# Kernel optimization log

Measured on AMD Instinct MI355X. Metric: run time of the kernel, lower is better.

## Reference

```python
import jax, jax.numpy as jnp
import numpy as np

WINDOW = 12  # fixed half-window from the original module


def setup_inputs() -> dict:
    key = jax.random.key(0)
    ks = jax.random.split(key, 8)
    B, S, G, H = 8, 512, 16, 128
    Da, Dm = 8 * H, 2 * H
    att = jax.random.normal(ks[0], (B, S, Da), jnp.float32)
    mod = jax.random.normal(ks[1], (B, S, Dm), jnp.float32)
    W_att = jax.random.normal(ks[2], (3 * Da,), jnp.float32) * 0.02
    b_att = jax.random.normal(ks[3], (1,), jnp.float32) * 0.02
    W_mod = jax.random.normal(ks[4], (3 * Dm,), jnp.float32) * 0.02
    b_mod = jax.random.normal(ks[5], (1,), jnp.float32) * 0.02
    q_enc = jax.random.normal(ks[6], (B, 30, Dm), jnp.float32)
    gap_indices = jax.random.randint(ks[7], (B, G), 0, S)
    mask = jnp.ones((B, S), jnp.int32)
    q_mask = jnp.ones((B, 30), jnp.int32)
    return dict(att=att, mod=mod, W_att=W_att, b_att=b_att, W_mod=W_mod,
                b_mod=b_mod, q_enc=q_enc, gap_indices=gap_indices,
                mask=mask, q_mask=q_mask)


def _pools(x, maskf, wmf):
    # x: [B,S,D]; maskf: [B,S] float; wmf: [B,G-1,S] float window masks
    # gap 0: full-sequence pooling (max is unmasked, avg divides by mask sum -- faithful)
    max0 = jnp.max(x, axis=1)                                   # [B,D]
    avg0 = jnp.sum(x, axis=1) / jnp.sum(maskf, axis=1, keepdims=True)
    p0 = jnp.concatenate([max0, avg0], axis=-1)[:, None, :]      # [B,1,2D]
    # remaining gaps: masked windowed max/avg (masked entries zeroed, as in torch)
    s = jnp.einsum('bgs,bsd->bgd', wmf, x)                       # windowed sums
    cnt = jnp.sum(wmf, axis=2, keepdims=True)                    # [B,G-1,1]
    avg = s / cnt
    mx = jnp.max(x[:, None, :, :] * wmf[:, :, :, None], axis=2)  # [B,G-1,D]
    return jnp.concatenate([p0, jnp.concatenate([mx, avg], axis=-1)], axis=1)


def reference(att, mod, W_att, b_att, W_mod, b_mod, q_enc, gap_indices, mask, q_mask):
    B, S, _ = mod.shape
    bidx = jnp.arange(B)[:, None]
    att_gaps = att[bidx, gap_indices]   # [B,G,Da]
    mod_gaps = mod[bidx, gap_indices]   # [B,G,Dm]

    maskf = mask.astype(jnp.float32)
    gaps_rest = gap_indices[:, 1:]      # [B,G-1]
    idx = jnp.arange(S)
    wm = ((idx[None, None, :] >= gaps_rest[:, :, None] - WINDOW)
          & (idx[None, None, :] <= gaps_rest[:, :, None] + WINDOW)
          & (mask[:, None, :] > 0))
    wmf = wm.astype(jnp.float32)        # [B,G-1,S]

    pools_att = _pools(att, maskf, wmf)  # [B,G,2*Da]
    pools_mod = _pools(mod, maskf, wmf)  # [B,G,2*Dm]

    att_cat = jnp.concatenate([att_gaps, pools_att], axis=-1)  # [B,G,3*Da]
    mod_cat = jnp.concatenate([mod_gaps, pools_mod], axis=-1)  # [B,G,3*Dm]

    logits = (jnp.einsum('bgd,d->bg', att_cat, W_att) + b_att
              + jnp.einsum('bgd,d->bg', mod_cat, W_mod) + b_mod)
    return logits  # [B,G]
```

## Files before the change

### kernel.cpp

```cpp
#include <hip/hip_runtime.h>
#include <math.h>

#define B 8
#define S 512
#define G 16
#define DA 1024
#define DM 256
#define WIN 12
#define NCH 32
#define RPC (S / NCH)
#define DTOT (DA + DM)
#define NW 8
#define RPW (RPC / NW)

__inline__ __device__ float4 fmax4(float4 a, float4 b) {
    return make_float4(fmaxf(a.x, b.x), fmaxf(a.y, b.y),
                       fmaxf(a.z, b.z), fmaxf(a.w, b.w));
}
__inline__ __device__ float4 add4(float4 a, float4 b) {
    return make_float4(a.x + b.x, a.y + b.y, a.z + b.z, a.w + b.w);
}
__inline__ __device__ float dot4(float4 a, float4 b) {
    return a.x * b.x + a.y * b.y + a.z * b.z + a.w * b.w;
}

__inline__ __device__ float4 blockReduceSum4_8(float4 v, float4* sh) {
    int lane = threadIdx.x & 63, w = threadIdx.x >> 6;
#pragma unroll
    for (int o = 32; o > 0; o >>= 1) {
        v.x += __shfl_xor(v.x, o, 64);
        v.y += __shfl_xor(v.y, o, 64);
        v.z += __shfl_xor(v.z, o, 64);
        v.w += __shfl_xor(v.w, o, 64);
    }
    __syncthreads();
    if (lane == 0) sh[w] = v;
    __syncthreads();
    float4 r = sh[0];
#pragma unroll
    for (int ww = 1; ww < 8; ++ww) {
        r.x += sh[ww].x; r.y += sh[ww].y; r.z += sh[ww].z; r.w += sh[ww].w;
    }
    return r;
}

__global__ __launch_bounds__(512) void k_sweep(
    const float* __restrict__ att, const float* __restrict__ mod,
    float* __restrict__ pmax, float* __restrict__ psum)
{
    __shared__ float partM[NW][DTOT];
    __shared__ float partS[NW][DTOT];
    const int ch = blockIdx.x, b = blockIdx.y;
    const int t = threadIdx.x, lane = t & 63, w = t >> 6;

    const float4* att4 = (const float4*)att;
    const float4* mod4 = (const float4*)mod;

    float4 amax[4], asum[4];
#pragma unroll
    for (int k = 0; k < 4; ++k) {
        amax[k] = make_float4(-INFINITY, -INFINITY, -INFINITY, -INFINITY);
        asum[k] = make_float4(0.f, 0.f, 0.f, 0.f);
    }
    float4 mmax = make_float4(-INFINITY, -INFINITY, -INFINITY, -INFINITY);
    float4 msum = make_float4(0.f, 0.f, 0.f, 0.f);

    const int row0 = b * S + ch * RPC + w * RPW;
#pragma unroll
    for (int r = 0; r < RPW; ++r) {
        const float4* arow = att4 + (size_t)(row0 + r) * (DA / 4);
#pragma unroll
        for (int k = 0; k < 4; ++k) {
            float4 v = arow[lane + 64 * k];
            amax[k] = fmax4(amax[k], v);
            asum[k] = add4(asum[k], v);
        }
        float4 vm = mod4[(size_t)(row0 + r) * (DM / 4) + lane];
        mmax = fmax4(mmax, vm);
        msum = add4(msum, vm);
    }

    float4* pm = (float4*)&partM[w][0];
    float4* ps = (float4*)&partS[w][0];
#pragma unroll
    for (int k = 0; k < 4; ++k) {
        pm[lane + 64 * k] = amax[k];
        ps[lane + 64 * k] = asum[k];
    }
    ((float4*)&partM[w][DA])[lane] = mmax;
    ((float4*)&partS[w][DA])[lane] = msum;
    __syncthreads();

    const size_t base = ((size_t)b * NCH + ch) * DTOT;
    for (int d = t; d < DTOT; d += 512) {
        float mx = partM[0][d], sm = partS[0][d];
#pragma unroll
        for (int ww = 1; ww < NW; ++ww) {
            mx = fmaxf(mx, partM[ww][d]);
            sm += partS[ww][d];
        }
        pmax[base + d] = mx;
        psum[base + d] = sm;
    }
}

__global__ __launch_bounds__(512) void k_logits(
    const float* __restrict__ att, const float* __restrict__ mod,
    const float* __restrict__ Wa, const float* __restrict__ Wm,
    const float* __restrict__ ba, const float* __restrict__ bm,
    const int* __restrict__ gidx, const int* __restrict__ mask,
    const float* __restrict__ pmax, const float* __restrict__ psum,
    float* __restrict__ out)
{
    __shared__ float part[8][DTOT];
    __shared__ float4 s4[8];
    const int g = blockIdx.x, b = blockIdx.y;
    const int t = threadIdx.x, lane = t & 63, w = t >> 6;
    const int gi = gidx[b * G + g];

    const float4* att4 = (const float4*)att;
    const float4* mod4 = (const float4*)mod;

    float cd = 0.f;
    if (t < 256)
        cd = dot4(att4[(size_t)(b * S + gi) * (DA / 4) + t],
                  ((const float4*)Wa)[t]);
    else if (t < 256 + DM / 4)
        cd = dot4(mod4[(size_t)(b * S + gi) * (DM / 4) + (t - 256)],
                  ((const float4*)Wm)[t - 256]);

    if (g == 0) {
        float gd1 = 0.f, gd2 = 0.f;
        for (int d = t; d < DTOT; d += 512) {
            float mx = -INFINITY, sm = 0.f;
#pragma unroll 8
            for (int ch = 0; ch < NCH; ++ch) {
                const size_t o = ((size_t)b * NCH + ch) * DTOT + d;
                mx = fmaxf(mx, pmax[o]);
                sm += psum[o];
            }
            float wg1 = (d < DA) ? Wa[DA + d] : Wm[DM + (d - DA)];
            float wg2 = (d < DA) ? Wa[2 * DA + d] : Wm[2 * DM + (d - DA)];
            gd1 += wg1 * mx;
            gd2 += wg2 * sm;
        }
        float cm = 0.f;
        for (int s = t; s < S; s += 512) cm += (float)mask[b * S + s];

        float4 r = blockReduceSum4_8(make_float4(gd1, gd2, cd, cm), s4);
        if (t == 0)
            out[b * G + 0] = r.z + r.x + r.y / r.w + ba[0] + bm[0];
    } else {
        int lo = gi - WIN; if (lo < 0) lo = 0;
        int hi = gi + WIN; if (hi > S - 1) hi = S - 1;

        float4 amax2[4], asum2[4];
#pragma unroll
        for (int k = 0; k < 4; ++k) {
            amax2[k] = make_float4(0.f, 0.f, 0.f, 0.f);
            asum2[k] = make_float4(0.f, 0.f, 0.f, 0.f);
        }
        float4 mmax2 = make_float4(0.f, 0.f, 0.f, 0.f);
        float4 msum2 = make_float4(0.f, 0.f, 0.f, 0.f);
        float cn = 0.f;

        for (int s = lo + w; s <= hi; s += 8) {
            if (mask[b * S + s] > 0) {
                const int row = b * S + s;
                const float4* arow = att4 + (size_t)row * (DA / 4);
#pragma unroll
                for (int k = 0; k < 4; ++k) {
                    float4 v = arow[lane + 64 * k];
                    amax2[k] = fmax4(amax2[k], v);
                    asum2[k] = add4(asum2[k], v);
                }
                float4 vm = mod4[(size_t)row * (DM / 4) + lane];
                mmax2 = fmax4(mmax2, vm);
                msum2 = add4(msum2, vm);
                if (lane == 0) cn += 1.f;
            }
        }

        float4* pr = (float4*)&part[w][0];

#pragma unroll
        for (int k = 0; k < 4; ++k) pr[lane + 64 * k] = amax2[k];
        ((float4*)&part[w][DA])[lane] = mmax2;
        __syncthreads();
        float wdot1 = 0.f;
        for (int d = t; d < DTOT; d += 512) {
            float mx = part[0][d];
#pragma unroll
            for (int ww = 1; ww < 8; ++ww) mx = fmaxf(mx, part[ww][d]);
            float wgt = (d < DA) ? Wa[DA + d] : Wm[DM + (d - DA)];
            wdot1 += wgt * mx;
        }
        __syncthreads();

#pragma unroll
        for (int k = 0; k < 4; ++k) pr[lane + 64 * k] = asum2[k];
        ((float4*)&part[w][DA])[lane] = msum2;
        __syncthreads();
        float wdot2 = 0.f;
        for (int d = t; d < DTOT; d += 512) {
            float sm = part[0][d];
#pragma unroll
            for (int ww = 1; ww < 8; ++ww) sm += part[ww][d];
            float wgt = (d < DA) ? Wa[2 * DA + d] : Wm[2 * DM + (d - DA)];
            wdot2 += wgt * sm;
        }

        float4 r = blockReduceSum4_8(make_float4(wdot1, wdot2, cd, cn), s4);
        if (t == 0)
            out[b * G + g] = r.z + r.x + r.y / r.w + ba[0] + bm[0];
    }
}

extern "C" void kernel_launch(void* const* d_in, const int* in_sizes, int n_in,
                              void* d_out, int out_size, void* d_ws, size_t ws_size,
                              hipStream_t stream) {
    const float* att  = (const float*)d_in[0];
    const float* mod  = (const float*)d_in[1];
    const float* Wa   = (const float*)d_in[2];
    const float* ba   = (const float*)d_in[3];
    const float* Wm   = (const float*)d_in[4];
    const float* bm   = (const float*)d_in[5];
    const int* gidx   = (const int*)d_in[7];
    const int* mask   = (const int*)d_in[8];
    float* out = (float*)d_out;

    float* ws   = (float*)d_ws;
    float* pmax = ws;
    float* psum = pmax + (size_t)B * NCH * DTOT;

    k_sweep<<<dim3(NCH, B), 512, 0, stream>>>(att, mod, pmax, psum);
    k_logits<<<dim3(G, B), 512, 0, stream>>>(att, mod, Wa, Wm, ba, bm,
                                             gidx, mask, pmax, psum, out);
}
```

Measured before the change: 19.20 us.

## Merge sweep and window blocks into one launch, parallelize gap-0 reduction

The full-sequence sweep blocks and the windowed-gap blocks (gaps 1..15) now run in one kernel launch, so the window work overlaps the sweep instead of waiting for it. The former serial gap-0 reduction done by a single block per batch becomes a separate kernel with 21 blocks per batch that each reduce a 64-column slice of the chunk partials and atomically add into the output. A memset zeroes the output first. This adds a memset launch and nondeterministic float atomic ordering, and the sweep blocks now use a single shared buffer with an extra barrier.

```diff
diff --git a/kernel.cpp b/kernel.cpp
--- a/kernel.cpp
+++ b/kernel.cpp
@@ -12,6 +12,8 @@
 #define DTOT (DA + DM)
 #define NW 8
 #define RPW (RPC / NW)
+#define NWIN (B * (G - 1))
+#define NBLK1 (NWIN + NCH * B)
 
 __inline__ __device__ float4 fmax4(float4 a, float4 b) {
     return make_float4(fmaxf(a.x, b.x), fmaxf(a.y, b.y),
@@ -44,113 +46,87 @@
     return r;
 }
 
-__global__ __launch_bounds__(512) void k_sweep(
-    const float* __restrict__ att, const float* __restrict__ mod,
-    float* __restrict__ pmax, float* __restrict__ psum)
-{
-    __shared__ float partM[NW][DTOT];
-    __shared__ float partS[NW][DTOT];
-    const int ch = blockIdx.x, b = blockIdx.y;
-    const int t = threadIdx.x, lane = t & 63, w = t >> 6;
-
-    const float4* att4 = (const float4*)att;
-    const float4* mod4 = (const float4*)mod;
-
-    float4 amax[4], asum[4];
-#pragma unroll
-    for (int k = 0; k < 4; ++k) {
-        amax[k] = make_float4(-INFINITY, -INFINITY, -INFINITY, -INFINITY);
-        asum[k] = make_float4(0.f, 0.f, 0.f, 0.f);
-    }
-    float4 mmax = make_float4(-INFINITY, -INFINITY, -INFINITY, -INFINITY);
-    float4 msum = make_float4(0.f, 0.f, 0.f, 0.f);
-
-    const int row0 = b * S + ch * RPC + w * RPW;
-#pragma unroll
-    for (int r = 0; r < RPW; ++r) {
-        const float4* arow = att4 + (size_t)(row0 + r) * (DA / 4);
-#pragma unroll
-        for (int k = 0; k < 4; ++k) {
-            float4 v = arow[lane + 64 * k];
-            amax[k] = fmax4(amax[k], v);
-            asum[k] = add4(asum[k], v);
-        }
-        float4 vm = mod4[(size_t)(row0 + r) * (DM / 4) + lane];
-        mmax = fmax4(mmax, vm);
-        msum = add4(msum, vm);
-    }
-
-    float4* pm = (float4*)&partM[w][0];
-    float4* ps = (float4*)&partS[w][0];
-#pragma unroll
-    for (int k = 0; k < 4; ++k) {
-        pm[lane + 64 * k] = amax[k];
-        ps[lane + 64 * k] = asum[k];
-    }
-    ((float4*)&partM[w][DA])[lane] = mmax;
-    ((float4*)&partS[w][DA])[lane] = msum;
-    __syncthreads();
-
-    const size_t base = ((size_t)b * NCH + ch) * DTOT;
-    for (int d = t; d < DTOT; d += 512) {
-        float mx = partM[0][d], sm = partS[0][d];
-#pragma unroll
-        for (int ww = 1; ww < NW; ++ww) {
-            mx = fmaxf(mx, partM[ww][d]);
-            sm += partS[ww][d];
-        }
-        pmax[base + d] = mx;
-        psum[base + d] = sm;
-    }
-}
-
-__global__ __launch_bounds__(512) void k_logits(
+__global__ __launch_bounds__(512) void k_main(
     const float* __restrict__ att, const float* __restrict__ mod,
     const float* __restrict__ Wa, const float* __restrict__ Wm,
     const float* __restrict__ ba, const float* __restrict__ bm,
     const int* __restrict__ gidx, const int* __restrict__ mask,
-    const float* __restrict__ pmax, const float* __restrict__ psum,
+    float* __restrict__ pmax, float* __restrict__ psum,
     float* __restrict__ out)
 {
-    __shared__ float part[8][DTOT];
-    __shared__ float4 s4[8];
-    const int g = blockIdx.x, b = blockIdx.y;
+    __shared__ float part[NW][DTOT];
+    __shared__ float4 s4[NW];
+    const int bid = blockIdx.x;
     const int t = threadIdx.x, lane = t & 63, w = t >> 6;
-    const int gi = gidx[b * G + g];
 
     const float4* att4 = (const float4*)att;
     const float4* mod4 = (const float4*)mod;
 
-    float cd = 0.f;
-    if (t < 256)
-        cd = dot4(att4[(size_t)(b * S + gi) * (DA / 4) + t],
-                  ((const float4*)Wa)[t]);
-    else if (t < 256 + DM / 4)
-        cd = dot4(mod4[(size_t)(b * S + gi) * (DM / 4) + (t - 256)],
-                  ((const float4*)Wm)[t - 256]);
-
-    if (g == 0) {
-        float gd1 = 0.f, gd2 = 0.f;
-        for (int d = t; d < DTOT; d += 512) {
-            float mx = -INFINITY, sm = 0.f;
-#pragma unroll 8
-            for (int ch = 0; ch < NCH; ++ch) {
-                const size_t o = ((size_t)b * NCH + ch) * DTOT + d;
-                mx = fmaxf(mx, pmax[o]);
-                sm += psum[o];
+    if (bid >= NWIN) {
+        const int sid = bid - NWIN;
+        const int b = sid >> 5, ch = sid & (NCH - 1);
+
+        float4 amax[4], asum[4];
+#pragma unroll
+        for (int k = 0; k < 4; ++k) {
+            amax[k] = make_float4(-INFINITY, -INFINITY, -INFINITY, -INFINITY);
+            asum[k] = make_float4(0.f, 0.f, 0.f, 0.f);
+        }
+        float4 mmax = make_float4(-INFINITY, -INFINITY, -INFINITY, -INFINITY);
+        float4 msum = make_float4(0.f, 0.f, 0.f, 0.f);
+
+        const int row0 = b * S + ch * RPC + w * RPW;
+#pragma unroll
+        for (int r = 0; r < RPW; ++r) {
+            const float4* arow = att4 + (size_t)(row0 + r) * (DA / 4);
+#pragma unroll
+            for (int k = 0; k < 4; ++k) {
+                float4 v = arow[lane + 64 * k];
+                amax[k] = fmax4(amax[k], v);
+                asum[k] = add4(asum[k], v);
             }
-            float wg1 = (d < DA) ? Wa[DA + d] : Wm[DM + (d - DA)];
-            float wg2 = (d < DA) ? Wa[2 * DA + d] : Wm[2 * DM + (d - DA)];
-            gd1 += wg1 * mx;
-            gd2 += wg2 * sm;
-        }
-        float cm = 0.f;
-        for (int s = t; s < S; s += 512) cm += (float)mask[b * S + s];
-
-        float4 r = blockReduceSum4_8(make_float4(gd1, gd2, cd, cm), s4);
-        if (t == 0)
-            out[b * G + 0] = r.z + r.x + r.y / r.w + ba[0] + bm[0];
+            float4 vm = mod4[(size_t)(row0 + r) * (DM / 4) + lane];
+            mmax = fmax4(mmax, vm);
+            msum = add4(msum, vm);
+        }
+
+        const size_t base = ((size_t)b * NCH + ch) * DTOT;
+        float4* pr = (float4*)&part[w][0];
+
+#pragma unroll
+        for (int k = 0; k < 4; ++k) pr[lane + 64 * k] = amax[k];
+        ((float4*)&part[w][DA])[lane] = mmax;
+        __syncthreads();
+        for (int d = t; d < DTOT; d += 512) {
+            float mx = part[0][d];
+#pragma unroll
+            for (int ww = 1; ww < NW; ++ww) mx = fmaxf(mx, part[ww][d]);
+            pmax[base + d] = mx;
+        }
+        __syncthreads();
+
+#pragma unroll
+        for (int k = 0; k < 4; ++k) pr[lane + 64 * k] = asum[k];
+        ((float4*)&part[w][DA])[lane] = msum;
+        __syncthreads();
+        for (int d = t; d < DTOT; d += 512) {
+            float sm = part[0][d];
+#pragma unroll
+            for (int ww = 1; ww < NW; ++ww) sm += part[ww][d];
+            psum[base + d] = sm;
+        }
     } else {
+        const int b = bid / (G - 1), g = 1 + bid % (G - 1);
+        const int gi = gidx[b * G + g];
+
+        float cd = 0.f;
+        if (t < 256)
+            cd = dot4(att4[(size_t)(b * S + gi) * (DA / 4) + t],
+                      ((const float4*)Wa)[t]);
+        else if (t < 256 + DM / 4)
+            cd = dot4(mod4[(size_t)(b * S + gi) * (DM / 4) + (t - 256)],
+                      ((const float4*)Wm)[t - 256]);
+
         int lo = gi - WIN; if (lo < 0) lo = 0;
         int hi = gi + WIN; if (hi > S - 1) hi = S - 1;
 
@@ -164,7 +140,7 @@
         float4 msum2 = make_float4(0.f, 0.f, 0.f, 0.f);
         float cn = 0.f;
 
-        for (int s = lo + w; s <= hi; s += 8) {
+        for (int s = lo + w; s <= hi; s += NW) {
             if (mask[b * S + s] > 0) {
                 const int row = b * S + s;
                 const float4* arow = att4 + (size_t)row * (DA / 4);
@@ -213,6 +189,70 @@
         float4 r = blockReduceSum4_8(make_float4(wdot1, wdot2, cd, cn), s4);
         if (t == 0)
             out[b * G + g] = r.z + r.x + r.y / r.w + ba[0] + bm[0];
+    }
+}
+
+__global__ __launch_bounds__(512) void k_g0(
+    const float* __restrict__ att, const float* __restrict__ mod,
+    const float* __restrict__ Wa, const float* __restrict__ Wm,
+    const float* __restrict__ ba, const float* __restrict__ bm,
+    const int* __restrict__ gidx, const int* __restrict__ mask,
+    const float* __restrict__ pmax, const float* __restrict__ psum,
+    float* __restrict__ out)
+{
+    __shared__ float pM[NW][64], pS[NW][64];
+    __shared__ float4 s4[NW];
+    const int c = blockIdx.x, b = blockIdx.y;
+    const int t = threadIdx.x, lane = t & 63, w = t >> 6;
+
+    float cmv = (float)mask[b * S + t];
+    float cm = blockReduceSum4_8(make_float4(cmv, 0.f, 0.f, 0.f), s4).x;
+
+    if (c < 20) {
+        const int d = c * 64 + lane;
+        float mx = -INFINITY, sm = 0.f;
+#pragma unroll
+        for (int k = 0; k < NCH / NW; ++k) {
+            const int ch = w + NW * k;
+            const size_t o = ((size_t)b * NCH + ch) * DTOT + d;
+            mx = fmaxf(mx, pmax[o]);
+            sm += psum[o];
+        }
+        pM[w][lane] = mx;
+        pS[w][lane] = sm;
+        __syncthreads();
+
+        float val = 0.f;
+        if (t < 64) {
+            float m2 = pM[0][t], s2 = pS[0][t];
+#pragma unroll
+            for (int ww = 1; ww < NW; ++ww) {
+                m2 = fmaxf(m2, pM[ww][t]);
+                s2 += pS[ww][t];
+            }
+            const int d2 = c * 64 + t;
+            float w1 = (d2 < DA) ? Wa[DA + d2] : Wm[DM + (d2 - DA)];
+            float w2 = (d2 < DA) ? Wa[2 * DA + d2] : Wm[2 * DM + (d2 - DA)];
+            val = w1 * m2 + w2 * (s2 / cm);
+        }
+        if (w == 0) {
+#pragma unroll
+            for (int o = 32; o > 0; o >>= 1) val += __shfl_xor(val, o, 64);
+            if (lane == 0) atomicAdd(&out[b * G], val);
+        }
+    } else {
+        const int gi = gidx[b * G];
+        const float4* att4 = (const float4*)att;
+        const float4* mod4 = (const float4*)mod;
+        float cd = 0.f;
+        if (t < 256)
+            cd = dot4(att4[(size_t)(b * S + gi) * (DA / 4) + t],
+                      ((const float4*)Wa)[t]);
+        else if (t < 256 + DM / 4)
+            cd = dot4(mod4[(size_t)(b * S + gi) * (DM / 4) + (t - 256)],
+                      ((const float4*)Wm)[t - 256]);
+        float4 r = blockReduceSum4_8(make_float4(cd, 0.f, 0.f, 0.f), s4);
+        if (t == 0) atomicAdd(&out[b * G], r.x + ba[0] + bm[0]);
     }
 }
 
@@ -233,7 +273,9 @@
     float* pmax = ws;
     float* psum = pmax + (size_t)B * NCH * DTOT;
 
-    k_sweep<<<dim3(NCH, B), 512, 0, stream>>>(att, mod, pmax, psum);
-    k_logits<<<dim3(G, B), 512, 0, stream>>>(att, mod, Wa, Wm, ba, bm,
-                                             gidx, mask, pmax, psum, out);
-}
+    hipMemsetAsync(out, 0, (size_t)out_size * sizeof(float), stream);
+    k_main<<<NBLK1, 512, 0, stream>>>(att, mod, Wa, Wm, ba, bm, gidx, mask,
+                                      pmax, psum, out);
+    k_g0<<<dim3(21, B), 512, 0, stream>>>(att, mod, Wa, Wm, ba, bm, gidx, mask,
+                                          pmax, psum, out);
+}
```

Measured after the change: 21.41 us. 1.12x slower.
